# Performance work log

Hardware: AMD Instinct MI355X
Metric: run time of the kernel (lower is better)

The kernel has to match this reference:

```python
import jax, jax.numpy as jnp
import numpy as np

EPS = 1e-6


def setup_inputs() -> dict:
    key = jax.random.key(0)
    k1, k2, k3 = jax.random.split(key, 3)
    B, H, L, D = 1, 16, 1024, 64
    return {
        "q": jax.random.normal(k1, (B, H, L, D), dtype=jnp.float32),
        "k": jax.random.normal(k2, (B, H, L, D), dtype=jnp.float32),
        "v": jax.random.normal(k3, (B, H, L, D), dtype=jnp.float32),
    }


def reference(q, k, v):
    bsz, head_num, tgt_len, dim = q.shape
    src_len = k.shape[2]
    m = max(src_len, tgt_len)

    # flatten batch*heads: [N, L, D]
    q = jax.nn.relu(q.reshape(-1, tgt_len, dim))
    k = jax.nn.relu(k.reshape(-1, src_len, dim))
    v = v.reshape(-1, src_len, dim)

    # cosFormer re-weighting index: pi/2 * (1..m) / m, shape [1, m, 1]
    idx = (np.pi / 2) * jnp.arange(1, m + 1, dtype=q.dtype).reshape(1, -1, 1) / m
    sin_w = jnp.sin(idx)
    cos_w = jnp.cos(idx)

    # feature-mapped q/k: [N, L, 2D]
    q_ = jnp.concatenate([q * sin_w[:, :tgt_len, :], q * cos_w[:, :tgt_len, :]], axis=-1)
    k_ = jnp.concatenate([k * sin_w[:, :src_len, :], k * cos_w[:, :src_len, :]], axis=-1)

    # causal linear attention via cumulative outer products
    kv_ = jnp.einsum("nld,nlm->nldm", k_, v)          # [N, L, 2D, D]
    kv_cum = jnp.cumsum(kv_, axis=1)
    qkv = jnp.einsum("nld,nldm->nlm", q_, kv_cum)      # [N, L, D]

    k_cum = jnp.cumsum(k_, axis=1)                      # [N, L, 2D]
    denom = jnp.clip(jnp.einsum("nld,nld->nl", q_, k_cum), EPS, None)

    out = qkv / denom[..., None]
    return out.reshape(bsz, head_num, tgt_len, dim)
```

## Files before the change

### kernel.cpp

```cpp
#include <hip/hip_runtime.h>

namespace {
constexpr int Hh = 16;
constexpr int Ll = 1024;
constexpr int Dd = 64;
constexpr int Cc = 64;
constexpr int NCHUNK = Ll / Cc;
constexpr float PI_HALF = 1.5707963267948966f;
constexpr float EPSV = 1e-6f;
}

typedef __attribute__((ext_vector_type(8))) short short8;
typedef __attribute__((ext_vector_type(4))) float floatx4;

__device__ __forceinline__ unsigned short f2bf(float x) {
    unsigned int u = __float_as_uint(x);
    unsigned int r = u + 0x7fffu + ((u >> 16) & 1u);
    return (unsigned short)(r >> 16);
}

__global__ __launch_bounds__(256)
void cf_prep(const float* __restrict__ kin, const float* __restrict__ vin,
             unsigned short* __restrict__ kfT, unsigned short* __restrict__ vT) {
    const int jt = blockIdx.x, h = blockIdx.y;
    const int tid = threadIdx.x;
    constexpr int S1 = 72;
    __shared__ unsigned short AkT[128 * S1];
    __shared__ unsigned short Vt[64 * S1];

    const size_t gbase = ((size_t)h * Ll + (size_t)jt * Cc) * Dd;
    const float4* k4 = (const float4*)(kin + gbase);
    const float4* v4 = (const float4*)(vin + gbase);
    #pragma unroll
    for (int i = 0; i < 4; ++i) {
        int e4 = i * 256 + tid;
        int j = e4 >> 4, d4 = (e4 & 15) * 4;
        float th = PI_HALF * (float)(jt * Cc + j + 1) * (1.0f / (float)Ll);
        float sj, cj; __sincosf(th, &sj, &cj);
        float4 kx = k4[e4];
        float r0 = fmaxf(kx.x, 0.f), r1 = fmaxf(kx.y, 0.f);
        float r2 = fmaxf(kx.z, 0.f), r3 = fmaxf(kx.w, 0.f);
        AkT[(d4 + 0) * S1 + j] = f2bf(r0 * sj);
        AkT[(d4 + 1) * S1 + j] = f2bf(r1 * sj);
        AkT[(d4 + 2) * S1 + j] = f2bf(r2 * sj);
        AkT[(d4 + 3) * S1 + j] = f2bf(r3 * sj);
        AkT[(64 + d4 + 0) * S1 + j] = f2bf(r0 * cj);
        AkT[(64 + d4 + 1) * S1 + j] = f2bf(r1 * cj);
        AkT[(64 + d4 + 2) * S1 + j] = f2bf(r2 * cj);
        AkT[(64 + d4 + 3) * S1 + j] = f2bf(r3 * cj);
        float4 vx = v4[e4];
        Vt[(d4 + 0) * S1 + j] = f2bf(vx.x);
        Vt[(d4 + 1) * S1 + j] = f2bf(vx.y);
        Vt[(d4 + 2) * S1 + j] = f2bf(vx.z);
        Vt[(d4 + 3) * S1 + j] = f2bf(vx.w);
    }
    __syncthreads();

    unsigned short* kout = kfT + (size_t)h * 128 * Ll + jt * Cc;
    #pragma unroll
    for (int i = 0; i < 4; ++i) {
        int idx = i * 256 + tid;
        int row = idx >> 3, c8 = (idx & 7) * 8;
        *(uint4*)(kout + (size_t)row * Ll + c8) = *(const uint4*)&AkT[row * S1 + c8];
    }
    unsigned short* vout = vT + (size_t)h * 64 * Ll + jt * Cc;
    #pragma unroll
    for (int i = 0; i < 2; ++i) {
        int idx = i * 256 + tid;
        int row = idx >> 3, c8 = (idx & 7) * 8;
        *(uint4*)(vout + (size_t)row * Ll + c8) = *(const uint4*)&Vt[row * S1 + c8];
    }
}

__global__ __launch_bounds__(256)
void cf_main(const float* __restrict__ qin, const float* __restrict__ kin,
             const unsigned short* __restrict__ kfT,
             const unsigned short* __restrict__ vT,
             float* __restrict__ out) {
    const int c = blockIdx.x, h = blockIdx.y;
    const int tid = threadIdx.x;
    constexpr int SA = 200, SB = 136, SV = 200;
    __shared__ unsigned short Aq[64 * SA];
    __shared__ unsigned short Bk[80 * SB];
    __shared__ unsigned short Bv[64 * SV];

    const int wave = tid >> 6, lane = tid & 63;
    const int lrow = lane & 15, quad = lane >> 4;

    #pragma unroll
    for (int i = 0; i < 4; ++i) {
        int z = i * 256 + tid;
        if (z < 1020) ((unsigned int*)Bk)[(65 * SB) / 2 + z] = 0u;
    }

    floatx4 acc[2][5];
    #pragma unroll
    for (int t = 0; t < 2; ++t)
        #pragma unroll
        for (int nt = 0; nt < 5; ++nt)
            acc[t][nt] = (floatx4){0.f, 0.f, 0.f, 0.f};

    const unsigned short* At = kfT + (size_t)h * 128 * Ll;
    const unsigned short* Bt = vT + (size_t)h * 64 * Ll;
    short8 bones;
    {
        short o = (lrow == 0) ? (short)0x3F80 : (short)0;
        #pragma unroll
        for (int i = 0; i < 8; ++i) bones[i] = o;
    }
    const int nk = c * Cc;
    const int a0 = (wave * 32 + lrow) * Ll + quad * 8;
    const int a1 = a0 + 16 * Ll;
    const int br0 = (0 * 16 + lrow) * Ll + quad * 8;
    const int br1 = (1 * 16 + lrow) * Ll + quad * 8;
    const int br2 = (2 * 16 + lrow) * Ll + quad * 8;
    const int br3 = (3 * 16 + lrow) * Ll + quad * 8;

    if (nk > 0) {
        short8 af0 = *(const short8*)(At + a0);
        short8 af1 = *(const short8*)(At + a1);
        short8 vb0 = *(const short8*)(Bt + br0);
        short8 vb1 = *(const short8*)(Bt + br1);
        short8 vb2 = *(const short8*)(Bt + br2);
        short8 vb3 = *(const short8*)(Bt + br3);
        for (int kk = 0; kk < nk; kk += 32) {
            const int nx = kk + 32;
            short8 naf0 = af0, naf1 = af1;
            short8 nb0 = vb0, nb1 = vb1, nb2 = vb2, nb3 = vb3;
            if (nx < nk) {
                naf0 = *(const short8*)(At + a0 + nx);
                naf1 = *(const short8*)(At + a1 + nx);
                nb0 = *(const short8*)(Bt + br0 + nx);
                nb1 = *(const short8*)(Bt + br1 + nx);
                nb2 = *(const short8*)(Bt + br2 + nx);
                nb3 = *(const short8*)(Bt + br3 + nx);
            }
            acc[0][0] = __builtin_amdgcn_mfma_f32_16x16x32_bf16(af0, vb0, acc[0][0], 0, 0, 0);
            acc[0][1] = __builtin_amdgcn_mfma_f32_16x16x32_bf16(af0, vb1, acc[0][1], 0, 0, 0);
            acc[0][2] = __builtin_amdgcn_mfma_f32_16x16x32_bf16(af0, vb2, acc[0][2], 0, 0, 0);
            acc[0][3] = __builtin_amdgcn_mfma_f32_16x16x32_bf16(af0, vb3, acc[0][3], 0, 0, 0);
            acc[0][4] = __builtin_amdgcn_mfma_f32_16x16x32_bf16(af0, bones, acc[0][4], 0, 0, 0);
            acc[1][0] = __builtin_amdgcn_mfma_f32_16x16x32_bf16(af1, vb0, acc[1][0], 0, 0, 0);
            acc[1][1] = __builtin_amdgcn_mfma_f32_16x16x32_bf16(af1, vb1, acc[1][1], 0, 0, 0);
            acc[1][2] = __builtin_amdgcn_mfma_f32_16x16x32_bf16(af1, vb2, acc[1][2], 0, 0, 0);
            acc[1][3] = __builtin_amdgcn_mfma_f32_16x16x32_bf16(af1, vb3, acc[1][3], 0, 0, 0);
            acc[1][4] = __builtin_amdgcn_mfma_f32_16x16x32_bf16(af1, bones, acc[1][4], 0, 0, 0);
            af0 = naf0; af1 = naf1;
            vb0 = nb0; vb1 = nb1; vb2 = nb2; vb3 = nb3;
        }
    }

    const size_t gbase = ((size_t)h * Ll + (size_t)c * Cc) * Dd;
    const float4* q4 = (const float4*)(qin + gbase);
    const float4* k4 = (const float4*)(kin + gbase);
    #pragma unroll
    for (int i = 0; i < 4; ++i) {
        int e4 = i * 256 + tid;
        int j = e4 >> 4, d4 = (e4 & 15) * 4;
        float th = PI_HALF * (float)(c * Cc + j + 1) * (1.0f / (float)Ll);
        float sj, cj; __sincosf(th, &sj, &cj);
        float4 qv = q4[e4];
        float q0 = fmaxf(qv.x, 0.f), q1 = fmaxf(qv.y, 0.f);
        float q2 = fmaxf(qv.z, 0.f), q3 = fmaxf(qv.w, 0.f);
        *(ushort4*)&Aq[j * SA + 64 + d4] =
            make_ushort4(f2bf(q0 * sj), f2bf(q1 * sj), f2bf(q2 * sj), f2bf(q3 * sj));
        *(ushort4*)&Aq[j * SA + 128 + d4] =
            make_ushort4(f2bf(q0 * cj), f2bf(q1 * cj), f2bf(q2 * cj), f2bf(q3 * cj));
        float4 kx = k4[e4];
        float k0 = fmaxf(kx.x, 0.f), k1 = fmaxf(kx.y, 0.f);
        float k2 = fmaxf(kx.z, 0.f), k3 = fmaxf(kx.w, 0.f);
        *(ushort4*)&Bk[j * SB + d4] =
            make_ushort4(f2bf(k0 * sj), f2bf(k1 * sj), f2bf(k2 * sj), f2bf(k3 * sj));
        *(ushort4*)&Bk[j * SB + 64 + d4] =
            make_ushort4(f2bf(k0 * cj), f2bf(k1 * cj), f2bf(k2 * cj), f2bf(k3 * cj));
    }
    const unsigned short* vsrc = Bt + c * Cc;
    #pragma unroll
    for (int i = 0; i < 2; ++i) {
        int idx = i * 256 + tid;
        int d = idx >> 3, j8 = (idx & 7) * 8;
        *(uint4*)&Bv[d * SV + j8] = *(const uint4*)(vsrc + (size_t)d * Ll + j8);
    }
    #pragma unroll
    for (int t = 0; t < 2; ++t) {
        const int ft = wave * 2 + t;
        #pragma unroll
        for (int nt = 0; nt < 4; ++nt) {
            *(ushort4*)&Bv[(nt * 16 + lrow) * SV + 64 + ft * 16 + quad * 4] =
                make_ushort4(f2bf(acc[t][nt][0]), f2bf(acc[t][nt][1]),
                             f2bf(acc[t][nt][2]), f2bf(acc[t][nt][3]));
        }
        if (lrow == 0)
            *(ushort4*)&Bk[64 * SB + ft * 16 + quad * 4] =
                make_ushort4(f2bf(acc[t][4][0]), f2bf(acc[t][4][1]),
                             f2bf(acc[t][4][2]), f2bf(acc[t][4][3]));
    }
    __syncthreads();

    const int l0 = wave * 16;
    const int arow = (l0 + lrow) * SA;

    short8 a1f[4];
    #pragma unroll
    for (int ks = 0; ks < 4; ++ks)
        a1f[ks] = *(const short8*)&Aq[arow + 64 + ks * 32 + quad * 8];
    floatx4 rs = {0.f, 0.f, 0.f, 0.f};
    #pragma unroll
    for (int nt = 0; nt < 5; ++nt) {
        floatx4 sc = {0.f, 0.f, 0.f, 0.f};
        #pragma unroll
        for (int ks = 0; ks < 4; ++ks) {
            short8 bf = *(const short8*)&Bk[(nt * 16 + lrow) * SB + ks * 32 + quad * 8];
            sc = __builtin_amdgcn_mfma_f32_16x16x32_bf16(a1f[ks], bf, sc, 0, 0, 0);
        }
        if (nt < 4) {
            int j = nt * 16 + lrow;
            #pragma unroll
            for (int r = 0; r < 4; ++r) {
                int l = l0 + quad * 4 + r;
                float m = (j <= l) ? sc[r] : 0.f;
                sc[r] = m;
                Aq[l * SA + j] = f2bf(m);
            }
        }
        rs += sc;
    }
    #pragma unroll
    for (int m = 1; m <= 8; m <<= 1) {
        rs[0] += __shfl_xor(rs[0], m);
        rs[1] += __shfl_xor(rs[1], m);
        rs[2] += __shfl_xor(rs[2], m);
        rs[3] += __shfl_xor(rs[3], m);
    }
    float inv[4];
    #pragma unroll
    for (int r = 0; r < 4; ++r) inv[r] = 1.0f / fmaxf(rs[r], EPSV);

    __syncthreads();

    short8 sc0 = *(const short8*)&Aq[arow + 0 * 32 + quad * 8];
    short8 sc1 = *(const short8*)&Aq[arow + 1 * 32 + quad * 8];
    #pragma unroll
    for (int nt = 0; nt < 4; ++nt) {
        const int brow = (nt * 16 + lrow) * SV;
        floatx4 oacc = {0.f, 0.f, 0.f, 0.f};
        short8 b0 = *(const short8*)&Bv[brow + 0 * 32 + quad * 8];
        oacc = __builtin_amdgcn_mfma_f32_16x16x32_bf16(sc0, b0, oacc, 0, 0, 0);
        short8 b1 = *(const short8*)&Bv[brow + 1 * 32 + quad * 8];
        oacc = __builtin_amdgcn_mfma_f32_16x16x32_bf16(sc1, b1, oacc, 0, 0, 0);
        #pragma unroll
        for (int ks = 2; ks < 6; ++ks) {
            short8 bf = *(const short8*)&Bv[brow + ks * 32 + quad * 8];
            oacc = __builtin_amdgcn_mfma_f32_16x16x32_bf16(a1f[ks - 2], bf, oacc, 0, 0, 0);
        }
        #pragma unroll
        for (int r = 0; r < 4; ++r) {
            int l = l0 + quad * 4 + r;
            out[gbase + (size_t)l * Dd + nt * 16 + lrow] = oacc[r] * inv[r];
        }
    }
}

extern "C" void kernel_launch(void* const* d_in, const int* in_sizes, int n_in,
                              void* d_out, int out_size, void* d_ws, size_t ws_size,
                              hipStream_t stream) {
    const float* q = (const float*)d_in[0];
    const float* k = (const float*)d_in[1];
    const float* v = (const float*)d_in[2];
    float* out = (float*)d_out;
    unsigned short* kfT = (unsigned short*)d_ws;
    unsigned short* vT = kfT + (size_t)Hh * 128 * Ll;
    dim3 grid(NCHUNK, Hh);
    cf_prep<<<grid, 256, 0, stream>>>(k, v, kfT, vT);
    cf_main<<<grid, 256, 0, stream>>>(q, k, kfT, vT, out);
}
```

Measured before the change: 90.09 us.

## Split causal prefix reduction across two wave groups with 512-thread blocks

Doubles the main kernel's block to 512 threads and splits the prefix KV accumulation over two wave groups that take alternating 32-column k slices. The partial sums are then combined through shared memory. The inner loop now prefetches two steps ahead, and the q/k/v chunk loads are issued before the reduction loop so their latency overlaps it. The cost is an extra shared-memory reduction, two more barriers, and half the waves sitting idle during the intra-chunk phase. The prefetch also reads up to 128 elements past nk, which may touch the next head's rows at the end of a row.

```diff
diff --git a/kernel.cpp b/kernel.cpp
--- a/kernel.cpp
+++ b/kernel.cpp
@@ -72,7 +72,7 @@
     }
 }
 
-__global__ __launch_bounds__(256)
+__global__ __launch_bounds__(512)
 void cf_main(const float* __restrict__ qin, const float* __restrict__ kin,
              const unsigned short* __restrict__ kfT,
              const unsigned short* __restrict__ vT,
@@ -80,18 +80,26 @@
     const int c = blockIdx.x, h = blockIdx.y;
     const int tid = threadIdx.x;
     constexpr int SA = 200, SB = 136, SV = 200;
-    __shared__ unsigned short Aq[64 * SA];
-    __shared__ unsigned short Bk[80 * SB];
-    __shared__ unsigned short Bv[64 * SV];
+    __shared__ unsigned short SM[64 * SA + 80 * SB + 64 * SV];
+    unsigned short* Aq = SM;
+    unsigned short* Bk = SM + 64 * SA;
+    unsigned short* Bv = SM + 64 * SA + 80 * SB;
+    float* red = (float*)SM;
 
     const int wave = tid >> 6, lane = tid & 63;
     const int lrow = lane & 15, quad = lane >> 4;
-
-    #pragma unroll
-    for (int i = 0; i < 4; ++i) {
-        int z = i * 256 + tid;
-        if (z < 1020) ((unsigned int*)Bk)[(65 * SB) / 2 + z] = 0u;
-    }
+    const int wavef = wave & 3, waveK = wave >> 2;
+
+    const unsigned short* At = kfT + (size_t)h * 128 * Ll;
+    const unsigned short* Bt = vT + (size_t)h * 64 * Ll;
+    const size_t gbase = ((size_t)h * Ll + (size_t)c * Cc) * Dd;
+
+    const float4* q4 = (const float4*)(qin + gbase);
+    const float4* k4 = (const float4*)(kin + gbase);
+    float4 qr[2], kr[2];
+    qr[0] = q4[tid]; qr[1] = q4[512 + tid];
+    kr[0] = k4[tid]; kr[1] = k4[512 + tid];
+    uint4 vr = *(const uint4*)(Bt + c * Cc + (size_t)(tid >> 3) * Ll + (tid & 7) * 8);
 
     floatx4 acc[2][5];
     #pragma unroll
@@ -100,8 +108,6 @@
         for (int nt = 0; nt < 5; ++nt)
             acc[t][nt] = (floatx4){0.f, 0.f, 0.f, 0.f};
 
-    const unsigned short* At = kfT + (size_t)h * 128 * Ll;
-    const unsigned short* Bt = vT + (size_t)h * 64 * Ll;
     short8 bones;
     {
         short o = (lrow == 0) ? (short)0x3F80 : (short)0;
@@ -109,64 +115,91 @@
         for (int i = 0; i < 8; ++i) bones[i] = o;
     }
     const int nk = c * Cc;
-    const int a0 = (wave * 32 + lrow) * Ll + quad * 8;
+    const int a0 = (wavef * 32 + lrow) * Ll + quad * 8;
     const int a1 = a0 + 16 * Ll;
-    const int br0 = (0 * 16 + lrow) * Ll + quad * 8;
-    const int br1 = (1 * 16 + lrow) * Ll + quad * 8;
-    const int br2 = (2 * 16 + lrow) * Ll + quad * 8;
-    const int br3 = (3 * 16 + lrow) * Ll + quad * 8;
-
-    if (nk > 0) {
-        short8 af0 = *(const short8*)(At + a0);
-        short8 af1 = *(const short8*)(At + a1);
-        short8 vb0 = *(const short8*)(Bt + br0);
-        short8 vb1 = *(const short8*)(Bt + br1);
-        short8 vb2 = *(const short8*)(Bt + br2);
-        short8 vb3 = *(const short8*)(Bt + br3);
-        for (int kk = 0; kk < nk; kk += 32) {
-            const int nx = kk + 32;
-            short8 naf0 = af0, naf1 = af1;
-            short8 nb0 = vb0, nb1 = vb1, nb2 = vb2, nb3 = vb3;
-            if (nx < nk) {
-                naf0 = *(const short8*)(At + a0 + nx);
-                naf1 = *(const short8*)(At + a1 + nx);
-                nb0 = *(const short8*)(Bt + br0 + nx);
-                nb1 = *(const short8*)(Bt + br1 + nx);
-                nb2 = *(const short8*)(Bt + br2 + nx);
-                nb3 = *(const short8*)(Bt + br3 + nx);
-            }
-            acc[0][0] = __builtin_amdgcn_mfma_f32_16x16x32_bf16(af0, vb0, acc[0][0], 0, 0, 0);
-            acc[0][1] = __builtin_amdgcn_mfma_f32_16x16x32_bf16(af0, vb1, acc[0][1], 0, 0, 0);
-            acc[0][2] = __builtin_amdgcn_mfma_f32_16x16x32_bf16(af0, vb2, acc[0][2], 0, 0, 0);
-            acc[0][3] = __builtin_amdgcn_mfma_f32_16x16x32_bf16(af0, vb3, acc[0][3], 0, 0, 0);
-            acc[0][4] = __builtin_amdgcn_mfma_f32_16x16x32_bf16(af0, bones, acc[0][4], 0, 0, 0);
-            acc[1][0] = __builtin_amdgcn_mfma_f32_16x16x32_bf16(af1, vb0, acc[1][0], 0, 0, 0);
-            acc[1][1] = __builtin_amdgcn_mfma_f32_16x16x32_bf16(af1, vb1, acc[1][1], 0, 0, 0);
-            acc[1][2] = __builtin_amdgcn_mfma_f32_16x16x32_bf16(af1, vb2, acc[1][2], 0, 0, 0);
-            acc[1][3] = __builtin_amdgcn_mfma_f32_16x16x32_bf16(af1, vb3, acc[1][3], 0, 0, 0);
-            acc[1][4] = __builtin_amdgcn_mfma_f32_16x16x32_bf16(af1, bones, acc[1][4], 0, 0, 0);
-            af0 = naf0; af1 = naf1;
-            vb0 = nb0; vb1 = nb1; vb2 = nb2; vb3 = nb3;
-        }
-    }
-
-    const size_t gbase = ((size_t)h * Ll + (size_t)c * Cc) * Dd;
-    const float4* q4 = (const float4*)(qin + gbase);
-    const float4* k4 = (const float4*)(kin + gbase);
-    #pragma unroll
-    for (int i = 0; i < 4; ++i) {
-        int e4 = i * 256 + tid;
+    const int br0 = lrow * Ll + quad * 8;
+    const int br1 = br0 + 16 * Ll;
+    const int br2 = br0 + 32 * Ll;
+    const int br3 = br0 + 48 * Ll;
+
+    int kk = waveK * 32;
+    if (kk < nk) {
+        short8 Aa0 = *(const short8*)(At + a0 + kk);
+        short8 Aa1 = *(const short8*)(At + a1 + kk);
+        short8 Ab0 = *(const short8*)(Bt + br0 + kk);
+        short8 Ab1 = *(const short8*)(Bt + br1 + kk);
+        short8 Ab2 = *(const short8*)(Bt + br2 + kk);
+        short8 Ab3 = *(const short8*)(Bt + br3 + kk);
+        short8 Ba0 = *(const short8*)(At + a0 + kk + 64);
+        short8 Ba1 = *(const short8*)(At + a1 + kk + 64);
+        short8 Bb0 = *(const short8*)(Bt + br0 + kk + 64);
+        short8 Bb1 = *(const short8*)(Bt + br1 + kk + 64);
+        short8 Bb2 = *(const short8*)(Bt + br2 + kk + 64);
+        short8 Bb3 = *(const short8*)(Bt + br3 + kk + 64);
+        for (; kk < nk; kk += 64) {
+            short8 Ca0 = *(const short8*)(At + a0 + kk + 128);
+            short8 Ca1 = *(const short8*)(At + a1 + kk + 128);
+            short8 Cb0 = *(const short8*)(Bt + br0 + kk + 128);
+            short8 Cb1 = *(const short8*)(Bt + br1 + kk + 128);
+            short8 Cb2 = *(const short8*)(Bt + br2 + kk + 128);
+            short8 Cb3 = *(const short8*)(Bt + br3 + kk + 128);
+            acc[0][0] = __builtin_amdgcn_mfma_f32_16x16x32_bf16(Aa0, Ab0, acc[0][0], 0, 0, 0);
+            acc[0][1] = __builtin_amdgcn_mfma_f32_16x16x32_bf16(Aa0, Ab1, acc[0][1], 0, 0, 0);
+            acc[0][2] = __builtin_amdgcn_mfma_f32_16x16x32_bf16(Aa0, Ab2, acc[0][2], 0, 0, 0);
+            acc[0][3] = __builtin_amdgcn_mfma_f32_16x16x32_bf16(Aa0, Ab3, acc[0][3], 0, 0, 0);
+            acc[0][4] = __builtin_amdgcn_mfma_f32_16x16x32_bf16(Aa0, bones, acc[0][4], 0, 0, 0);
+            acc[1][0] = __builtin_amdgcn_mfma_f32_16x16x32_bf16(Aa1, Ab0, acc[1][0], 0, 0, 0);
+            acc[1][1] = __builtin_amdgcn_mfma_f32_16x16x32_bf16(Aa1, Ab1, acc[1][1], 0, 0, 0);
+            acc[1][2] = __builtin_amdgcn_mfma_f32_16x16x32_bf16(Aa1, Ab2, acc[1][2], 0, 0, 0);
+            acc[1][3] = __builtin_amdgcn_mfma_f32_16x16x32_bf16(Aa1, Ab3, acc[1][3], 0, 0, 0);
+            acc[1][4] = __builtin_amdgcn_mfma_f32_16x16x32_bf16(Aa1, bones, acc[1][4], 0, 0, 0);
+            Aa0 = Ba0; Aa1 = Ba1; Ab0 = Bb0; Ab1 = Bb1; Ab2 = Bb2; Ab3 = Bb3;
+            Ba0 = Ca0; Ba1 = Ca1; Bb0 = Cb0; Bb1 = Cb1; Bb2 = Cb2; Bb3 = Cb3;
+        }
+    }
+
+    if (waveK == 1) {
+        float* r = red + (wavef * 64 + lane) * 41;
+        #pragma unroll
+        for (int t = 0; t < 2; ++t)
+            #pragma unroll
+            for (int nt = 0; nt < 5; ++nt)
+                #pragma unroll
+                for (int rr = 0; rr < 4; ++rr)
+                    r[t * 20 + nt * 4 + rr] = acc[t][nt][rr];
+    }
+    __syncthreads();
+    if (waveK == 0) {
+        const float* r = red + (wavef * 64 + lane) * 41;
+        #pragma unroll
+        for (int t = 0; t < 2; ++t)
+            #pragma unroll
+            for (int nt = 0; nt < 5; ++nt)
+                #pragma unroll
+                for (int rr = 0; rr < 4; ++rr)
+                    acc[t][nt][rr] += r[t * 20 + nt * 4 + rr];
+    }
+    __syncthreads();
+
+    #pragma unroll
+    for (int i = 0; i < 2; ++i) {
+        int z = i * 512 + tid;
+        if (z < 1020) ((unsigned int*)Bk)[(65 * SB) / 2 + z] = 0u;
+    }
+    #pragma unroll
+    for (int i = 0; i < 2; ++i) {
+        int e4 = i * 512 + tid;
         int j = e4 >> 4, d4 = (e4 & 15) * 4;
         float th = PI_HALF * (float)(c * Cc + j + 1) * (1.0f / (float)Ll);
         float sj, cj; __sincosf(th, &sj, &cj);
-        float4 qv = q4[e4];
+        float4 qv = qr[i];
         float q0 = fmaxf(qv.x, 0.f), q1 = fmaxf(qv.y, 0.f);
         float q2 = fmaxf(qv.z, 0.f), q3 = fmaxf(qv.w, 0.f);
         *(ushort4*)&Aq[j * SA + 64 + d4] =
             make_ushort4(f2bf(q0 * sj), f2bf(q1 * sj), f2bf(q2 * sj), f2bf(q3 * sj));
         *(ushort4*)&Aq[j * SA + 128 + d4] =
             make_ushort4(f2bf(q0 * cj), f2bf(q1 * cj), f2bf(q2 * cj), f2bf(q3 * cj));
-        float4 kx = k4[e4];
+        float4 kx = kr[i];
         float k0 = fmaxf(kx.x, 0.f), k1 = fmaxf(kx.y, 0.f);
         float k2 = fmaxf(kx.z, 0.f), k3 = fmaxf(kx.w, 0.f);
         *(ushort4*)&Bk[j * SB + d4] =
@@ -174,89 +207,88 @@
         *(ushort4*)&Bk[j * SB + 64 + d4] =
             make_ushort4(f2bf(k0 * cj), f2bf(k1 * cj), f2bf(k2 * cj), f2bf(k3 * cj));
     }
-    const unsigned short* vsrc = Bt + c * Cc;
-    #pragma unroll
-    for (int i = 0; i < 2; ++i) {
-        int idx = i * 256 + tid;
-        int d = idx >> 3, j8 = (idx & 7) * 8;
-        *(uint4*)&Bv[d * SV + j8] = *(const uint4*)(vsrc + (size_t)d * Ll + j8);
-    }
-    #pragma unroll
-    for (int t = 0; t < 2; ++t) {
-        const int ft = wave * 2 + t;
+    *(uint4*)&Bv[(tid >> 3) * SV + (tid & 7) * 8] = vr;
+
+    if (waveK == 0) {
+        #pragma unroll
+        for (int t = 0; t < 2; ++t) {
+            const int ft = wavef * 2 + t;
+            #pragma unroll
+            for (int nt = 0; nt < 4; ++nt) {
+                *(ushort4*)&Bv[(nt * 16 + lrow) * SV + 64 + ft * 16 + quad * 4] =
+                    make_ushort4(f2bf(acc[t][nt][0]), f2bf(acc[t][nt][1]),
+                                 f2bf(acc[t][nt][2]), f2bf(acc[t][nt][3]));
+            }
+            if (lrow == 0)
+                *(ushort4*)&Bk[64 * SB + ft * 16 + quad * 4] =
+                    make_ushort4(f2bf(acc[t][4][0]), f2bf(acc[t][4][1]),
+                                 f2bf(acc[t][4][2]), f2bf(acc[t][4][3]));
+        }
+    }
+    __syncthreads();
+
+    const int l0 = wavef * 16;
+    const int arow = (l0 + lrow) * SA;
+    short8 a1f[4];
+    float inv[4];
+    if (waveK == 0) {
+        #pragma unroll
+        for (int ks = 0; ks < 4; ++ks)
+            a1f[ks] = *(const short8*)&Aq[arow + 64 + ks * 32 + quad * 8];
+        floatx4 rs = {0.f, 0.f, 0.f, 0.f};
+        #pragma unroll
+        for (int nt = 0; nt < 5; ++nt) {
+            floatx4 sc = {0.f, 0.f, 0.f, 0.f};
+            #pragma unroll
+            for (int ks = 0; ks < 4; ++ks) {
+                short8 bf = *(const short8*)&Bk[(nt * 16 + lrow) * SB + ks * 32 + quad * 8];
+                sc = __builtin_amdgcn_mfma_f32_16x16x32_bf16(a1f[ks], bf, sc, 0, 0, 0);
+            }
+            if (nt < 4) {
+                int j = nt * 16 + lrow;
+                #pragma unroll
+                for (int r = 0; r < 4; ++r) {
+                    int l = l0 + quad * 4 + r;
+                    float m = (j <= l) ? sc[r] : 0.f;
+                    sc[r] = m;
+                    Aq[l * SA + j] = f2bf(m);
+                }
+            }
+            rs += sc;
+        }
+        #pragma unroll
+        for (int m = 1; m <= 8; m <<= 1) {
+            rs[0] += __shfl_xor(rs[0], m);
+            rs[1] += __shfl_xor(rs[1], m);
+            rs[2] += __shfl_xor(rs[2], m);
+            rs[3] += __shfl_xor(rs[3], m);
+        }
+        #pragma unroll
+        for (int r = 0; r < 4; ++r) inv[r] = 1.0f / fmaxf(rs[r], EPSV);
+    }
+    __syncthreads();
+
+    if (waveK == 0) {
+        short8 sc0 = *(const short8*)&Aq[arow + 0 * 32 + quad * 8];
+        short8 sc1 = *(const short8*)&Aq[arow + 1 * 32 + quad * 8];
         #pragma unroll
         for (int nt = 0; nt < 4; ++nt) {
-            *(ushort4*)&Bv[(nt * 16 + lrow) * SV + 64 + ft * 16 + quad * 4] =
-                make_ushort4(f2bf(acc[t][nt][0]), f2bf(acc[t][nt][1]),
-                             f2bf(acc[t][nt][2]), f2bf(acc[t][nt][3]));
-        }
-        if (lrow == 0)
-            *(ushort4*)&Bk[64 * SB + ft * 16 + quad * 4] =
-                make_ushort4(f2bf(acc[t][4][0]), f2bf(acc[t][4][1]),
-                             f2bf(acc[t][4][2]), f2bf(acc[t][4][3]));
-    }
-    __syncthreads();
-
-    const int l0 = wave * 16;
-    const int arow = (l0 + lrow) * SA;
-
-    short8 a1f[4];
-    #pragma unroll
-    for (int ks = 0; ks < 4; ++ks)
-        a1f[ks] = *(const short8*)&Aq[arow + 64 + ks * 32 + quad * 8];
-    floatx4 rs = {0.f, 0.f, 0.f, 0.f};
-    #pragma unroll
-    for (int nt = 0; nt < 5; ++nt) {
-        floatx4 sc = {0.f, 0.f, 0.f, 0.f};
-        #pragma unroll
-        for (int ks = 0; ks < 4; ++ks) {
-            short8 bf = *(const short8*)&Bk[(nt * 16 + lrow) * SB + ks * 32 + quad * 8];
-            sc = __builtin_amdgcn_mfma_f32_16x16x32_bf16(a1f[ks], bf, sc, 0, 0, 0);
-        }
-        if (nt < 4) {
-            int j = nt * 16 + lrow;
+            const int brow = (nt * 16 + lrow) * SV;
+            floatx4 oacc = {0.f, 0.f, 0.f, 0.f};
+            short8 b0 = *(const short8*)&Bv[brow + 0 * 32 + quad * 8];
+            oacc = __builtin_amdgcn_mfma_f32_16x16x32_bf16(sc0, b0, oacc, 0, 0, 0);
+            short8 b1 = *(const short8*)&Bv[brow + 1 * 32 + quad * 8];
+            oacc = __builtin_amdgcn_mfma_f32_16x16x32_bf16(sc1, b1, oacc, 0, 0, 0);
+            #pragma unroll
+            for (int ks = 2; ks < 6; ++ks) {
+                short8 bf = *(const short8*)&Bv[brow + ks * 32 + quad * 8];
+                oacc = __builtin_amdgcn_mfma_f32_16x16x32_bf16(a1f[ks - 2], bf, oacc, 0, 0, 0);
+            }
             #pragma unroll
             for (int r = 0; r < 4; ++r) {
                 int l = l0 + quad * 4 + r;
-                float m = (j <= l) ? sc[r] : 0.f;
-                sc[r] = m;
-                Aq[l * SA + j] = f2bf(m);
-            }
-        }
-        rs += sc;
-    }
-    #pragma unroll
-    for (int m = 1; m <= 8; m <<= 1) {
-        rs[0] += __shfl_xor(rs[0], m);
-        rs[1] += __shfl_xor(rs[1], m);
-        rs[2] += __shfl_xor(rs[2], m);
-        rs[3] += __shfl_xor(rs[3], m);
-    }
-    float inv[4];
-    #pragma unroll
-    for (int r = 0; r < 4; ++r) inv[r] = 1.0f / fmaxf(rs[r], EPSV);
-
-    __syncthreads();
-
-    short8 sc0 = *(const short8*)&Aq[arow + 0 * 32 + quad * 8];
-    short8 sc1 = *(const short8*)&Aq[arow + 1 * 32 + quad * 8];
-    #pragma unroll
-    for (int nt = 0; nt < 4; ++nt) {
-        const int brow = (nt * 16 + lrow) * SV;
-        floatx4 oacc = {0.f, 0.f, 0.f, 0.f};
-        short8 b0 = *(const short8*)&Bv[brow + 0 * 32 + quad * 8];
-        oacc = __builtin_amdgcn_mfma_f32_16x16x32_bf16(sc0, b0, oacc, 0, 0, 0);
-        short8 b1 = *(const short8*)&Bv[brow + 1 * 32 + quad * 8];
-        oacc = __builtin_amdgcn_mfma_f32_16x16x32_bf16(sc1, b1, oacc, 0, 0, 0);
-        #pragma unroll
-        for (int ks = 2; ks < 6; ++ks) {
-            short8 bf = *(const short8*)&Bv[brow + ks * 32 + quad * 8];
-            oacc = __builtin_amdgcn_mfma_f32_16x16x32_bf16(a1f[ks - 2], bf, oacc, 0, 0, 0);
-        }
-        #pragma unroll
-        for (int r = 0; r < 4; ++r) {
-            int l = l0 + quad * 4 + r;
-            out[gbase + (size_t)l * Dd + nt * 16 + lrow] = oacc[r] * inv[r];
+                out[gbase + (size_t)l * Dd + nt * 16 + lrow] = oacc[r] * inv[r];
+            }
         }
     }
 }
@@ -272,5 +304,5 @@
     unsigned short* vT = kfT + (size_t)Hh * 128 * Ll;
     dim3 grid(NCHUNK, Hh);
     cf_prep<<<grid, 256, 0, stream>>>(k, v, kfT, vT);
-    cf_main<<<grid, 256, 0, stream>>>(q, k, kfT, vT, out);
-}
+    cf_main<<<grid, 512, 0, stream>>>(q, k, kfT, vT, out);
+}
```

Result: slower. 92.38 us (+2.5%).

## Stage prefix KV tiles through LDS with triple-buffered async global_load_lds

Applied to the files above, without the earlier changes.

Replaces direct register loads of the transposed K-feature and V tiles in the prefix-state accumulation loop with a three-stage LDS pipeline. Tiles are loaded asynchronously via global_load_lds using an XOR-swizzled layout, and waits are bounded by vmcnt so two tiles stay in flight during MFMA work. This targets global memory latency in the long causal prefix loop, where later blocks scan up to 1024 positions. The cost is an extra 72KB of shared memory, which lowers occupancy, plus a workgroup barrier on every tile.

```diff
diff --git a/kernel.cpp b/kernel.cpp
--- a/kernel.cpp
+++ b/kernel.cpp
@@ -18,6 +18,15 @@
     unsigned int r = u + 0x7fffu + ((u >> 16) & 1u);
     return (unsigned short)(r >> 16);
 }
+
+typedef __attribute__((address_space(3))) unsigned int lds_u32_t;
+typedef __attribute__((address_space(1))) unsigned int glb_u32_t;
+
+__device__ __forceinline__ void gld16(const unsigned short* g, unsigned short* l) {
+    __builtin_amdgcn_global_load_lds((const glb_u32_t*)g, (lds_u32_t*)l, 16, 0, 0);
+}
+
+#define MFMA16(a, b, c) __builtin_amdgcn_mfma_f32_16x16x32_bf16((a), (b), (c), 0, 0, 0)
 
 __global__ __launch_bounds__(256)
 void cf_prep(const float* __restrict__ kin, const float* __restrict__ vin,
@@ -83,6 +92,7 @@
     __shared__ unsigned short Aq[64 * SA];
     __shared__ unsigned short Bk[80 * SB];
     __shared__ unsigned short Bv[64 * SV];
+    __shared__ unsigned short Sta[3][192 * 64];
 
     const int wave = tid >> 6, lane = tid & 63;
     const int lrow = lane & 15, quad = lane >> 4;
@@ -108,45 +118,64 @@
         #pragma unroll
         for (int i = 0; i < 8; ++i) bones[i] = o;
     }
-    const int nk = c * Cc;
-    const int a0 = (wave * 32 + lrow) * Ll + quad * 8;
-    const int a1 = a0 + 16 * Ll;
-    const int br0 = (0 * 16 + lrow) * Ll + quad * 8;
-    const int br1 = (1 * 16 + lrow) * Ll + quad * 8;
-    const int br2 = (2 * 16 + lrow) * Ll + quad * 8;
-    const int br3 = (3 * 16 + lrow) * Ll + quad * 8;
-
-    if (nk > 0) {
-        short8 af0 = *(const short8*)(At + a0);
-        short8 af1 = *(const short8*)(At + a1);
-        short8 vb0 = *(const short8*)(Bt + br0);
-        short8 vb1 = *(const short8*)(Bt + br1);
-        short8 vb2 = *(const short8*)(Bt + br2);
-        short8 vb3 = *(const short8*)(Bt + br3);
-        for (int kk = 0; kk < nk; kk += 32) {
-            const int nx = kk + 32;
-            short8 naf0 = af0, naf1 = af1;
-            short8 nb0 = vb0, nb1 = vb1, nb2 = vb2, nb3 = vb3;
-            if (nx < nk) {
-                naf0 = *(const short8*)(At + a0 + nx);
-                naf1 = *(const short8*)(At + a1 + nx);
-                nb0 = *(const short8*)(Bt + br0 + nx);
-                nb1 = *(const short8*)(Bt + br1 + nx);
-                nb2 = *(const short8*)(Bt + br2 + nx);
-                nb3 = *(const short8*)(Bt + br3 + nx);
+
+    auto STAGE = [&](int buf, int tile) {
+        const int kk = tile * 64;
+        unsigned short* SA_ = &Sta[buf][0];
+        unsigned short* SB_ = &Sta[buf][128 * 64];
+        #pragma unroll
+        for (int i = 0; i < 4; ++i) {
+            int g = i * 256 + tid;
+            int r = g >> 3, cb = g & 7;
+            gld16(At + (size_t)r * Ll + kk + ((cb ^ (r & 7)) << 3), SA_ + g * 8);
+        }
+        #pragma unroll
+        for (int i = 0; i < 2; ++i) {
+            int g = i * 256 + tid;
+            int r = g >> 3, cb = g & 7;
+            gld16(Bt + (size_t)r * Ll + kk + ((cb ^ (r & 7)) << 3), SB_ + g * 8);
+        }
+    };
+    auto COMPUTE = [&](int buf) {
+        const unsigned short* SA_ = &Sta[buf][0];
+        const unsigned short* SB_ = &Sta[buf][128 * 64];
+        const int sw = lrow & 7;
+        const int r0 = wave * 32 + lrow, r1 = r0 + 16;
+        #pragma unroll
+        for (int ks = 0; ks < 2; ++ks) {
+            const int cb = ((ks * 4 + quad) ^ sw) << 3;
+            short8 a0 = *(const short8*)&SA_[r0 * 64 + cb];
+            short8 a1 = *(const short8*)&SA_[r1 * 64 + cb];
+            #pragma unroll
+            for (int nt = 0; nt < 4; ++nt) {
+                short8 b = *(const short8*)&SB_[(nt * 16 + lrow) * 64 + cb];
+                acc[0][nt] = MFMA16(a0, b, acc[0][nt]);
+                acc[1][nt] = MFMA16(a1, b, acc[1][nt]);
             }
-            acc[0][0] = __builtin_amdgcn_mfma_f32_16x16x32_bf16(af0, vb0, acc[0][0], 0, 0, 0);
-            acc[0][1] = __builtin_amdgcn_mfma_f32_16x16x32_bf16(af0, vb1, acc[0][1], 0, 0, 0);
-            acc[0][2] = __builtin_amdgcn_mfma_f32_16x16x32_bf16(af0, vb2, acc[0][2], 0, 0, 0);
-            acc[0][3] = __builtin_amdgcn_mfma_f32_16x16x32_bf16(af0, vb3, acc[0][3], 0, 0, 0);
-            acc[0][4] = __builtin_amdgcn_mfma_f32_16x16x32_bf16(af0, bones, acc[0][4], 0, 0, 0);
-            acc[1][0] = __builtin_amdgcn_mfma_f32_16x16x32_bf16(af1, vb0, acc[1][0], 0, 0, 0);
-            acc[1][1] = __builtin_amdgcn_mfma_f32_16x16x32_bf16(af1, vb1, acc[1][1], 0, 0, 0);
-            acc[1][2] = __builtin_amdgcn_mfma_f32_16x16x32_bf16(af1, vb2, acc[1][2], 0, 0, 0);
-            acc[1][3] = __builtin_amdgcn_mfma_f32_16x16x32_bf16(af1, vb3, acc[1][3], 0, 0, 0);
-            acc[1][4] = __builtin_amdgcn_mfma_f32_16x16x32_bf16(af1, bones, acc[1][4], 0, 0, 0);
-            af0 = naf0; af1 = naf1;
-            vb0 = nb0; vb1 = nb1; vb2 = nb2; vb3 = nb3;
+            acc[0][4] = MFMA16(a0, bones, acc[0][4]);
+            acc[1][4] = MFMA16(a1, bones, acc[1][4]);
+        }
+    };
+
+    const int ntile = c;
+    if (ntile >= 1) {
+        STAGE(0, 0);
+        if (ntile >= 2) {
+            STAGE(1, 1);
+            asm volatile("s_waitcnt vmcnt(6)" ::: "memory");
+        } else {
+            asm volatile("s_waitcnt vmcnt(0)" ::: "memory");
+        }
+        __builtin_amdgcn_s_barrier();
+        asm volatile("" ::: "memory");
+        for (int t = 0; t < ntile; ++t) {
+            const bool more = (t + 2) < ntile;
+            if (more) STAGE((t + 2) % 3, t + 2);
+            COMPUTE(t % 3);
+            if (more) asm volatile("s_waitcnt vmcnt(6)" ::: "memory");
+            else      asm volatile("s_waitcnt vmcnt(0)" ::: "memory");
+            __builtin_amdgcn_s_barrier();
+            asm volatile("" ::: "memory");
         }
     }
 
@@ -211,7 +240,7 @@
         #pragma unroll
         for (int ks = 0; ks < 4; ++ks) {
             short8 bf = *(const short8*)&Bk[(nt * 16 + lrow) * SB + ks * 32 + quad * 8];
-            sc = __builtin_amdgcn_mfma_f32_16x16x32_bf16(a1f[ks], bf, sc, 0, 0, 0);
+            sc = MFMA16(a1f[ks], bf, sc);
         }
         if (nt < 4) {
             int j = nt * 16 + lrow;
@@ -245,13 +274,13 @@
         const int brow = (nt * 16 + lrow) * SV;
         floatx4 oacc = {0.f, 0.f, 0.f, 0.f};
         short8 b0 = *(const short8*)&Bv[brow + 0 * 32 + quad * 8];
-        oacc = __builtin_amdgcn_mfma_f32_16x16x32_bf16(sc0, b0, oacc, 0, 0, 0);
+        oacc = MFMA16(sc0, b0, oacc);
         short8 b1 = *(const short8*)&Bv[brow + 1 * 32 + quad * 8];
-        oacc = __builtin_amdgcn_mfma_f32_16x16x32_bf16(sc1, b1, oacc, 0, 0, 0);
+        oacc = MFMA16(sc1, b1, oacc);
         #pragma unroll
         for (int ks = 2; ks < 6; ++ks) {
             short8 bf = *(const short8*)&Bv[brow + ks * 32 + quad * 8];
-            oacc = __builtin_amdgcn_mfma_f32_16x16x32_bf16(a1f[ks - 2], bf, oacc, 0, 0, 0);
+            oacc = MFMA16(a1f[ks - 2], bf, oacc);
         }
         #pragma unroll
         for (int r = 0; r < 4; ++r) {
```

Result: faster. 83.46 us (-7.4%).
